# Performance work log

Measured on AMD Instinct MI355X. Metric: run time of the kernel, lower is better.

Reference implementation:

```python
import jax, jax.numpy as jnp
import numpy as np

N_EMBD = 1024
N_HEAD = 16
HEAD_DIM = N_EMBD // N_HEAD


def setup_inputs() -> dict:
    key = jax.random.key(0)
    ks = jax.random.split(key, 9)
    B, T, C = 4, 2048, N_EMBD
    s = 1.0 / np.sqrt(C)
    return {
        "x": jax.random.normal(ks[0], (B, T, C), dtype=jnp.float32),
        "Wq": jax.random.normal(ks[1], (C, C), dtype=jnp.float32) * s,
        "bq": jnp.zeros((C,), dtype=jnp.float32),
        "Wk": jax.random.normal(ks[2], (C, C), dtype=jnp.float32) * s,
        "bk": jnp.zeros((C,), dtype=jnp.float32),
        "Wv": jax.random.normal(ks[3], (C, C), dtype=jnp.float32) * s,
        "bv": jnp.zeros((C,), dtype=jnp.float32),
        "Wo": jax.random.normal(ks[4], (C, C), dtype=jnp.float32) * s,
        "bo": jnp.zeros((C,), dtype=jnp.float32),
    }


def reference(x, Wq, bq, Wk, bk, Wv, bv, Wo, bo):
    B, T, C = x.shape
    H, D = N_HEAD, HEAD_DIM
    # torch Linear: y = x @ W.T + b ; here W stored as (in, out) so y = x @ W + b
    q = (x @ Wq + bq).reshape(B, T, H, D).transpose(0, 2, 1, 3)  # [B,H,T,D]
    k = (x @ Wk + bk).reshape(B, T, H, D).transpose(0, 2, 1, 3)
    v = (x @ Wv + bv).reshape(B, T, H, D).transpose(0, 2, 1, 3)
    scores = jnp.einsum('bhqd,bhkd->bhqk', q, k) / jnp.sqrt(jnp.float32(D))
    causal = jnp.tril(jnp.ones((T, T), dtype=bool))  # [T,T]
    scores = jnp.where(causal[None, None, :, :], scores, -jnp.inf)
    weights = jax.nn.softmax(scores, axis=-1)
    # dropout disabled (eval mode / deterministic reference)
    out = jnp.einsum('bhqk,bhkd->bhqd', weights, v)  # [B,H,T,D]
    out = out.transpose(0, 2, 1, 3).reshape(B, T, C)
    return out @ Wo + bo
```

## Files before the change

kernel.cpp:

```cpp
#include <hip/hip_runtime.h>
#include <stdint.h>
#include <stddef.h>

#define NB 4
#define NT 2048
#define NC 1024
#define NH 16
#define ND 64
#define NM (NB*NT)
#define KVB 64

typedef __bf16 bf16_t;
typedef __attribute__((ext_vector_type(8)))  __bf16 bf16x8;
typedef __attribute__((ext_vector_type(4)))  __bf16 bf16x4;
typedef __attribute__((ext_vector_type(2)))  __bf16 bf16x2;
typedef __attribute__((ext_vector_type(4)))  float  f32x4;
typedef __attribute__((ext_vector_type(16))) float  f32x16;
typedef __attribute__((ext_vector_type(4)))  unsigned int u32x4;

#define QK_SCALE_LOG2E 0.18033688011112042f

__device__ __forceinline__ f32x4 mfma_bf16(bf16x8 a, bf16x8 b, f32x4 c) {
  return __builtin_amdgcn_mfma_f32_16x16x32_bf16(a, b, c, 0, 0, 0);
}
__device__ __forceinline__ f32x16 mfma32(bf16x8 a, bf16x8 b, f32x16 c) {
  return __builtin_amdgcn_mfma_f32_32x32x16_bf16(a, b, c, 0, 0, 0);
}

__device__ __forceinline__ void gld_lds16(const void* g, void* l) {
  __builtin_amdgcn_global_load_lds(
      (const __attribute__((address_space(1))) void*)g,
      (__attribute__((address_space(3))) void*)l, 16, 0, 0);
}

__device__ __forceinline__ unsigned int pack_bf16(float a, float b) {
  bf16x2 t; t[0] = (bf16_t)a; t[1] = (bf16_t)b;
  return __builtin_bit_cast(unsigned int, t);
}

#if __has_builtin(__builtin_amdgcn_permlane32_swap)
typedef __attribute__((ext_vector_type(2))) unsigned int u32x2;
__device__ __forceinline__ void plswap(unsigned int &a, unsigned int &b) {
  u32x2 r = __builtin_amdgcn_permlane32_swap(a, b, false, false);
  a = r[0]; b = r[1];
}
#else
__device__ __forceinline__ void plswap(unsigned int &a, unsigned int &b) {
  asm volatile("s_nop 1\n\tv_permlane32_swap_b32 %0, %1\n\ts_nop 1"
               : "+v"(a), "+v"(b));
}
#endif

__global__ __launch_bounds__(256) void cast_x_kernel(const float* __restrict__ x,
                                                     bf16_t* __restrict__ xb, int n4) {
  const int stride = gridDim.x * blockDim.x;
  for (int i = blockIdx.x * blockDim.x + threadIdx.x; i < n4; i += stride) {
    float4 v = reinterpret_cast<const float4*>(x)[i];
    bf16x4 o;
    o[0] = (bf16_t)v.x; o[1] = (bf16_t)v.y; o[2] = (bf16_t)v.z; o[3] = (bf16_t)v.w;
    reinterpret_cast<bf16x4*>(xb)[i] = o;
  }
}

__global__ __launch_bounds__(256) void transpose_cast_kernel(const float* __restrict__ W,
                                                             bf16_t* __restrict__ WT) {
  __shared__ float tile[32][33];
  const int t = threadIdx.x;
  const int tx = t & 31, ty = t >> 5;
  const int k0 = (blockIdx.x & 31) << 5;
  const int n0 = (blockIdx.x >> 5) << 5;
#pragma unroll
  for (int i = 0; i < 4; ++i)
    tile[ty + 8*i][tx] = W[(size_t)(k0 + ty + 8*i)*NC + n0 + tx];
  __syncthreads();
#pragma unroll
  for (int i = 0; i < 4; ++i)
    WT[(size_t)(n0 + ty + 8*i)*NC + k0 + tx] = (bf16_t)tile[tx][ty + 8*i];
}

template<int MODE>
__global__ __launch_bounds__(256) void gemm_bt_kernel(
    const bf16_t* __restrict__ A, const bf16_t* __restrict__ BT,
    int M, int N, int K,
    bf16_t* __restrict__ qo, bf16_t* __restrict__ ko, bf16_t* __restrict__ vo,
    const float* __restrict__ b0, const float* __restrict__ b1, const float* __restrict__ b2,
    float* __restrict__ outp, const float* __restrict__ bo)
{
  const int lane = threadIdx.x & 63;
  const int wv = threadIdx.x >> 6;
  const int wr = wv >> 1, wc = wv & 1;
  const int l15 = lane & 15, lg = lane >> 4;
  const int nbn = N >> 7;
  const int bm = blockIdx.x / nbn, bn = blockIdx.x % nbn;
  const int m0 = bm << 7, n0 = bn << 7;

  __shared__ char smem[32768];
  char* As = smem;
  char* Bs = smem + 16384;

  f32x4 acc[4][4] = {};

  const int nkt = K >> 6;
  for (int kt = 0; kt < nkt; ++kt) {
    const int k0 = kt << 6;
    __syncthreads();
#pragma unroll
    for (int i = 0; i < 4; ++i) {
      const int seg = i*4 + wv;
      const int lin = seg*64 + lane;
      const int row = lin >> 3;
      const int ch  = (lin & 7) ^ (row & 7);
      gld_lds16(A  + (size_t)(m0 + row)*K + k0 + (ch << 3), As + seg*1024);
      gld_lds16(BT + (size_t)(n0 + row)*K + k0 + (ch << 3), Bs + seg*1024);
    }
    __syncthreads();
#pragma unroll
    for (int ks = 0; ks < 2; ++ks) {
      bf16x8 af[4], bfr[4];
#pragma unroll
      for (int fr = 0; fr < 4; ++fr) {
        const int row = wr*64 + fr*16 + l15;
        const int ch  = (ks*4 + lg) ^ (row & 7);
        af[fr] = *reinterpret_cast<const bf16x8*>(As + row*128 + ch*16);
      }
#pragma unroll
      for (int fc = 0; fc < 4; ++fc) {
        const int row = wc*64 + fc*16 + l15;
        const int ch  = (ks*4 + lg) ^ (row & 7);
        bfr[fc] = *reinterpret_cast<const bf16x8*>(Bs + row*128 + ch*16);
      }
#pragma unroll
      for (int fr = 0; fr < 4; ++fr)
#pragma unroll
        for (int fc = 0; fc < 4; ++fc)
          acc[fr][fc] = mfma_bf16(af[fr], bfr[fc], acc[fr][fc]);
    }
  }

#pragma unroll
  for (int fr = 0; fr < 4; ++fr) {
#pragma unroll
    for (int fc = 0; fc < 4; ++fc) {
      const int mrow0 = m0 + wr*64 + fr*16 + (lg << 2);
      const int ncol  = n0 + wc*64 + fc*16 + l15;
      if (MODE == 0) {
        const int mat = ncol >> 10, c = ncol & 1023;
        const int h = c >> 6, d = c & 63;
        if (mat == 2) {
          const float bias = b2[c];
          bf16x4 ov;
#pragma unroll
          for (int r = 0; r < 4; ++r) ov[r] = (bf16_t)(acc[fr][fc][r] + bias);
          const int bb = mrow0 >> 11, tt = mrow0 & (NT - 1);
          *reinterpret_cast<bf16x4*>(vo + ((((size_t)bb*NH + h)*ND + d)*NT) + tt) = ov;
        } else {
          bf16_t* dst = (mat == 0) ? qo : ko;
          const float* bptr = (mat == 0) ? b0 : b1;
          const float bias = bptr[c];
          const float scl = (mat == 0) ? QK_SCALE_LOG2E : 1.0f;
#pragma unroll
          for (int r = 0; r < 4; ++r) {
            const int mm = mrow0 + r;
            const int bb = mm >> 11, tt = mm & (NT - 1);
            dst[((((size_t)bb*NH + h)*NT + tt) << 6) + d] =
                (bf16_t)((acc[fr][fc][r] + bias) * scl);
          }
        }
      } else {
        const float bias = bo[ncol];
#pragma unroll
        for (int r = 0; r < 4; ++r)
          outp[(size_t)(mrow0 + r)*N + ncol] = acc[fr][fc][r] + bias;
      }
    }
  }
}

__global__ __launch_bounds__(256) void attn_kernel(
    const bf16_t* __restrict__ q, const bf16_t* __restrict__ k, const bf16_t* __restrict__ vt,
    bf16_t* __restrict__ o)
{
  const int lane = threadIdx.x & 63;
  const int wv = threadIdx.x >> 6;
  const int l31 = lane & 31, h = lane >> 5;

  const int qblk = 15 - (blockIdx.x >> 6);
  const int bh   = blockIdx.x & 63;
  const int bb = bh >> 4, hh = bh & 15;
  const int q0 = qblk << 7;

  __shared__ char smem[4*8192];
  char* const ks0 = smem;
  char* const ks1 = smem + 8192;
  char* const vs0 = smem + 16384;
  char* const vs1 = smem + 24576;

  const size_t base = (size_t)bh * (NT * ND);
  const bf16_t* Kg = k  + base;
  const bf16_t* Vg = vt + base;

  const int q0w = q0 + wv*32;
  const int qg  = q0w + l31;

#pragma unroll
  for (int p = 0; p < 2; ++p) {
    const int seg = p*4 + wv, lin = seg*64 + lane;
    const int row = lin >> 3, ch = (lin & 7) ^ (row & 7);
    gld_lds16(Kg + (size_t)row*ND + (ch << 3), ks0 + seg*1024);
    gld_lds16(Vg + (size_t)row*NT + (ch << 3), vs0 + seg*1024);
  }

  bf16x8 qf[4];
  {
    const bf16_t* Qg = q + base + (size_t)qg*ND + 8*h;
#pragma unroll
    for (int ds = 0; ds < 4; ++ds)
      qf[ds] = *reinterpret_cast<const bf16x8*>(Qg + 16*ds);
  }

  bf16x8 ones8;
#pragma unroll
  for (int jj = 0; jj < 8; ++jj) ones8[jj] = (bf16_t)1.0f;

  f32x16 oc[2] = {};
  f32x16 lacc = {};

  const int nkv = 2*qblk + 2;

  for (int j = 0; j < nkv; ++j) {
    const int kt0 = j << 6;
    const bool cur1 = (j & 1) != 0;
    char* Kc = cur1 ? ks1 : ks0;
    char* Vc = cur1 ? vs1 : vs0;

    if (j + 1 < nkv) {
      char* Kn = cur1 ? ks0 : ks1;
      char* Vn = cur1 ? vs0 : vs1;
      const int nt0 = kt0 + KVB;
#pragma unroll
      for (int p = 0; p < 2; ++p) {
        const int seg = p*4 + wv, lin = seg*64 + lane;
        const int row = lin >> 3, ch = (lin & 7) ^ (row & 7);
        gld_lds16(Kg + (size_t)(nt0 + row)*ND + (ch << 3), Kn + seg*1024);
        gld_lds16(Vg + (size_t)row*NT + nt0 + (ch << 3), Vn + seg*1024);
      }
      asm volatile("s_waitcnt vmcnt(4)" ::: "memory");
    } else {
      asm volatile("s_waitcnt vmcnt(0)" ::: "memory");
    }
    __syncthreads();

    const bool active = (kt0 <= q0w + 31);
    if (active) {
      f32x16 st[2] = {};
      __builtin_amdgcn_s_setprio(1);
#pragma unroll
      for (int ds = 0; ds < 4; ++ds) {
#pragma unroll
        for (int kt = 0; kt < 2; ++kt) {
          const int row = kt*32 + l31;
          const int cl  = (2*ds + h) ^ (row & 7);
          const bf16x8 kfr = *reinterpret_cast<const bf16x8*>(Kc + row*128 + cl*16);
          st[kt] = mfma32(kfr, qf[ds], st[kt]);
        }
      }
      __builtin_amdgcn_s_setprio(0);

      const bool needmask = (kt0 + KVB - 1) > q0w;
      if (needmask) {
        const int qrel = qg - kt0 - 4*h;
#pragma unroll
        for (int kt = 0; kt < 2; ++kt)
#pragma unroll
          for (int r = 0; r < 16; ++r) {
            const int kc = (r & 3) + 8*(r >> 2) + 32*kt;
            st[kt][r] = (kc > qrel) ? 0.0f : exp2f(st[kt][r]);
          }
      } else {
#pragma unroll
        for (int kt = 0; kt < 2; ++kt)
#pragma unroll
          for (int r = 0; r < 16; ++r)
            st[kt][r] = exp2f(st[kt][r]);
      }

#pragma unroll
      for (int kt = 0; kt < 2; ++kt) {
#pragma unroll
        for (int g = 0; g < 2; ++g) {
          unsigned int wa = pack_bf16(st[kt][8*g + 0], st[kt][8*g + 1]);
          unsigned int wb = pack_bf16(st[kt][8*g + 2], st[kt][8*g + 3]);
          unsigned int wc = pack_bf16(st[kt][8*g + 4], st[kt][8*g + 5]);
          unsigned int wd = pack_bf16(st[kt][8*g + 6], st[kt][8*g + 7]);
          plswap(wa, wc);
          plswap(wb, wd);
          u32x4 pb; pb[0] = wa; pb[1] = wb; pb[2] = wc; pb[3] = wd;
          const bf16x8 pf = __builtin_bit_cast(bf16x8, pb);
          const int kg = 2*kt + g;
          __builtin_amdgcn_s_setprio(1);
          lacc = mfma32(ones8, pf, lacc);
#pragma unroll
          for (int da = 0; da < 2; ++da) {
            const int row = 32*da + l31;
            const int cl  = (2*kg + h) ^ (row & 7);
            const bf16x8 vf = *reinterpret_cast<const bf16x8*>(Vc + row*128 + cl*16);
            oc[da] = mfma32(vf, pf, oc[da]);
          }
          __builtin_amdgcn_s_setprio(0);
        }
      }
    }
    __syncthreads();
  }

  const float rl = 1.0f / lacc[0];
  bf16_t* orow = o + ((size_t)bb*NT + qg)*NC + hh*ND;
#pragma unroll
  for (int da = 0; da < 2; ++da) {
#pragma unroll
    for (int u = 0; u < 4; ++u) {
      bf16x4 ov;
#pragma unroll
      for (int jj = 0; jj < 4; ++jj) ov[jj] = (bf16_t)(oc[da][4*u + jj] * rl);
      *reinterpret_cast<bf16x4*>(orow + 32*da + 8*u + 4*h) = ov;
    }
  }
}

extern "C" void kernel_launch(void* const* d_in, const int* in_sizes, int n_in,
                              void* d_out, int out_size, void* d_ws, size_t ws_size,
                              hipStream_t stream) {
  (void)in_sizes; (void)n_in; (void)out_size;
  const float* x  = (const float*)d_in[0];
  const float* Wq = (const float*)d_in[1];
  const float* bq = (const float*)d_in[2];
  const float* Wk = (const float*)d_in[3];
  const float* bk = (const float*)d_in[4];
  const float* Wv = (const float*)d_in[5];
  const float* bv = (const float*)d_in[6];
  const float* Wo = (const float*)d_in[7];
  const float* bo = (const float*)d_in[8];
  float* out = (float*)d_out;

  const size_t off_xb    = 0;
  const size_t off_wqkvT = 16777216;
  const size_t off_woT   = 23068672;
  const size_t off_q     = 25165824;
  const size_t off_k     = 41943040;
  const size_t off_v     = 58720256;
  const size_t off_attn  = 75497472;
  const size_t need      = 92274688;
  if (ws_size < need) return;

  char* ws = (char*)d_ws;
  bf16_t* xb    = (bf16_t*)(ws + off_xb);
  bf16_t* wqkvT = (bf16_t*)(ws + off_wqkvT);
  bf16_t* woT   = (bf16_t*)(ws + off_woT);
  bf16_t* qb    = (bf16_t*)(ws + off_q);
  bf16_t* kb    = (bf16_t*)(ws + off_k);
  bf16_t* vtb   = (bf16_t*)(ws + off_v);
  bf16_t* attnb = (bf16_t*)(ws + off_attn);

  cast_x_kernel<<<dim3(2048), dim3(256), 0, stream>>>(x, xb, NM*NC/4);
  transpose_cast_kernel<<<dim3(1024), dim3(256), 0, stream>>>(Wq, wqkvT);
  transpose_cast_kernel<<<dim3(1024), dim3(256), 0, stream>>>(Wk, wqkvT + 1048576);
  transpose_cast_kernel<<<dim3(1024), dim3(256), 0, stream>>>(Wv, wqkvT + 2097152);
  transpose_cast_kernel<<<dim3(1024), dim3(256), 0, stream>>>(Wo, woT);

  gemm_bt_kernel<0><<<dim3(64*24), dim3(256), 0, stream>>>(
      xb, wqkvT, NM, 3*NC, NC, qb, kb, vtb, bq, bk, bv, nullptr, nullptr);

  attn_kernel<<<dim3(16*64), dim3(256), 0, stream>>>(qb, kb, vtb, attnb);

  gemm_bt_kernel<1><<<dim3(64*8), dim3(256), 0, stream>>>(
      attnb, woT, NM, NC, NC, nullptr, nullptr, nullptr, nullptr, nullptr, nullptr,
      out, bo);
}
```

Before: 191.0 us.

## Shrink attention blocks to 64 query rows with two waves and single barrier

```diff
diff --git a/kernel.cpp b/kernel.cpp
--- a/kernel.cpp
+++ b/kernel.cpp
@@ -176,18 +176,19 @@
   }
 }
 
-__global__ __launch_bounds__(256) void attn_kernel(
+__global__ __launch_bounds__(128) void attn_kernel(
     const bf16_t* __restrict__ q, const bf16_t* __restrict__ k, const bf16_t* __restrict__ vt,
     bf16_t* __restrict__ o)
 {
-  const int lane = threadIdx.x & 63;
-  const int wv = threadIdx.x >> 6;
-  const int l31 = lane & 31, h = lane >> 5;
-
-  const int qblk = 15 - (blockIdx.x >> 6);
+  const int tid  = threadIdx.x;
+  const int lane = tid & 63;
+  const int wv   = tid >> 6;
+  const int l31  = lane & 31, h = lane >> 5;
+
+  const int tile = 31 - (blockIdx.x >> 6);
   const int bh   = blockIdx.x & 63;
   const int bb = bh >> 4, hh = bh & 15;
-  const int q0 = qblk << 7;
+  const int q0 = tile << 6;
 
   __shared__ char smem[4*8192];
   char* const ks0 = smem;
@@ -202,12 +203,21 @@
   const int q0w = q0 + wv*32;
   const int qg  = q0w + l31;
 
-#pragma unroll
-  for (int p = 0; p < 2; ++p) {
-    const int seg = p*4 + wv, lin = seg*64 + lane;
-    const int row = lin >> 3, ch = (lin & 7) ^ (row & 7);
-    gld_lds16(Kg + (size_t)row*ND + (ch << 3), ks0 + seg*1024);
-    gld_lds16(Vg + (size_t)row*NT + (ch << 3), vs0 + seg*1024);
+  int offk[4], offv[4], segb[4];
+#pragma unroll
+  for (int p = 0; p < 4; ++p) {
+    const int c   = p*128 + tid;
+    const int row = c >> 3;
+    const int ch  = (c & 7) ^ (row & 7);
+    offk[p] = row*ND + (ch << 3);
+    offv[p] = row*NT + (ch << 3);
+    segb[p] = (p*2 + wv) * 1024;
+  }
+
+#pragma unroll
+  for (int p = 0; p < 4; ++p) {
+    gld_lds16(Kg + offk[p], ks0 + segb[p]);
+    gld_lds16(Vg + offv[p], vs0 + segb[p]);
   }
 
   bf16x8 qf[4];
@@ -225,92 +235,86 @@
   f32x16 oc[2] = {};
   f32x16 lacc = {};
 
-  const int nkv = 2*qblk + 2;
+  const int nkv = tile + 1;
 
   for (int j = 0; j < nkv; ++j) {
-    const int kt0 = j << 6;
     const bool cur1 = (j & 1) != 0;
-    char* Kc = cur1 ? ks1 : ks0;
-    char* Vc = cur1 ? vs1 : vs0;
+    char* const Kc = cur1 ? ks1 : ks0;
+    char* const Vc = cur1 ? vs1 : vs0;
+
+    asm volatile("s_waitcnt vmcnt(0)" ::: "memory");
+    __builtin_amdgcn_s_barrier();
+    __builtin_amdgcn_sched_barrier(0);
 
     if (j + 1 < nkv) {
-      char* Kn = cur1 ? ks0 : ks1;
-      char* Vn = cur1 ? vs0 : vs1;
-      const int nt0 = kt0 + KVB;
-#pragma unroll
-      for (int p = 0; p < 2; ++p) {
-        const int seg = p*4 + wv, lin = seg*64 + lane;
-        const int row = lin >> 3, ch = (lin & 7) ^ (row & 7);
-        gld_lds16(Kg + (size_t)(nt0 + row)*ND + (ch << 3), Kn + seg*1024);
-        gld_lds16(Vg + (size_t)row*NT + nt0 + (ch << 3), Vn + seg*1024);
-      }
-      asm volatile("s_waitcnt vmcnt(4)" ::: "memory");
+      char* const Kn = cur1 ? ks0 : ks1;
+      char* const Vn = cur1 ? vs0 : vs1;
+      const int kadv = (j + 1) * (KVB * ND);
+      const int vadv = (j + 1) * KVB;
+#pragma unroll
+      for (int p = 0; p < 4; ++p) {
+        gld_lds16(Kg + kadv + offk[p], Kn + segb[p]);
+        gld_lds16(Vg + vadv + offv[p], Vn + segb[p]);
+      }
+      __builtin_amdgcn_sched_barrier(0);
+    }
+
+    f32x16 st[2] = {};
+    __builtin_amdgcn_s_setprio(1);
+#pragma unroll
+    for (int ds = 0; ds < 4; ++ds) {
+#pragma unroll
+      for (int kt = 0; kt < 2; ++kt) {
+        const int row = kt*32 + l31;
+        const int cl  = (2*ds + h) ^ (row & 7);
+        const bf16x8 kfr = *reinterpret_cast<const bf16x8*>(Kc + row*128 + cl*16);
+        st[kt] = mfma32(kfr, qf[ds], st[kt]);
+      }
+    }
+    __builtin_amdgcn_s_setprio(0);
+
+    if (j == nkv - 1) {
+      const int qrel = qg - (j << 6) - 4*h;
+#pragma unroll
+      for (int kt = 0; kt < 2; ++kt)
+#pragma unroll
+        for (int r = 0; r < 16; ++r) {
+          const int kc = (r & 3) + 8*(r >> 2) + 32*kt;
+          st[kt][r] = (kc > qrel) ? 0.0f : exp2f(st[kt][r]);
+        }
     } else {
-      asm volatile("s_waitcnt vmcnt(0)" ::: "memory");
-    }
-    __syncthreads();
-
-    const bool active = (kt0 <= q0w + 31);
-    if (active) {
-      f32x16 st[2] = {};
-      __builtin_amdgcn_s_setprio(1);
-#pragma unroll
-      for (int ds = 0; ds < 4; ++ds) {
-#pragma unroll
-        for (int kt = 0; kt < 2; ++kt) {
-          const int row = kt*32 + l31;
-          const int cl  = (2*ds + h) ^ (row & 7);
-          const bf16x8 kfr = *reinterpret_cast<const bf16x8*>(Kc + row*128 + cl*16);
-          st[kt] = mfma32(kfr, qf[ds], st[kt]);
+#pragma unroll
+      for (int kt = 0; kt < 2; ++kt)
+#pragma unroll
+        for (int r = 0; r < 16; ++r)
+          st[kt][r] = exp2f(st[kt][r]);
+    }
+
+#pragma unroll
+    for (int kt = 0; kt < 2; ++kt) {
+#pragma unroll
+      for (int g = 0; g < 2; ++g) {
+        unsigned int wa = pack_bf16(st[kt][8*g + 0], st[kt][8*g + 1]);
+        unsigned int wb = pack_bf16(st[kt][8*g + 2], st[kt][8*g + 3]);
+        unsigned int wc = pack_bf16(st[kt][8*g + 4], st[kt][8*g + 5]);
+        unsigned int wd = pack_bf16(st[kt][8*g + 6], st[kt][8*g + 7]);
+        plswap(wa, wc);
+        plswap(wb, wd);
+        u32x4 pb; pb[0] = wa; pb[1] = wb; pb[2] = wc; pb[3] = wd;
+        const bf16x8 pf = __builtin_bit_cast(bf16x8, pb);
+        const int kg = 2*kt + g;
+        __builtin_amdgcn_s_setprio(1);
+        lacc = mfma32(ones8, pf, lacc);
+#pragma unroll
+        for (int da = 0; da < 2; ++da) {
+          const int row = 32*da + l31;
+          const int cl  = (2*kg + h) ^ (row & 7);
+          const bf16x8 vf = *reinterpret_cast<const bf16x8*>(Vc + row*128 + cl*16);
+          oc[da] = mfma32(vf, pf, oc[da]);
         }
-      }
-      __builtin_amdgcn_s_setprio(0);
-
-      const bool needmask = (kt0 + KVB - 1) > q0w;
-      if (needmask) {
-        const int qrel = qg - kt0 - 4*h;
-#pragma unroll
-        for (int kt = 0; kt < 2; ++kt)
-#pragma unroll
-          for (int r = 0; r < 16; ++r) {
-            const int kc = (r & 3) + 8*(r >> 2) + 32*kt;
-            st[kt][r] = (kc > qrel) ? 0.0f : exp2f(st[kt][r]);
-          }
-      } else {
-#pragma unroll
-        for (int kt = 0; kt < 2; ++kt)
-#pragma unroll
-          for (int r = 0; r < 16; ++r)
-            st[kt][r] = exp2f(st[kt][r]);
-      }
-
-#pragma unroll
-      for (int kt = 0; kt < 2; ++kt) {
-#pragma unroll
-        for (int g = 0; g < 2; ++g) {
-          unsigned int wa = pack_bf16(st[kt][8*g + 0], st[kt][8*g + 1]);
-          unsigned int wb = pack_bf16(st[kt][8*g + 2], st[kt][8*g + 3]);
-          unsigned int wc = pack_bf16(st[kt][8*g + 4], st[kt][8*g + 5]);
-          unsigned int wd = pack_bf16(st[kt][8*g + 6], st[kt][8*g + 7]);
-          plswap(wa, wc);
-          plswap(wb, wd);
-          u32x4 pb; pb[0] = wa; pb[1] = wb; pb[2] = wc; pb[3] = wd;
-          const bf16x8 pf = __builtin_bit_cast(bf16x8, pb);
-          const int kg = 2*kt + g;
-          __builtin_amdgcn_s_setprio(1);
-          lacc = mfma32(ones8, pf, lacc);
-#pragma unroll
-          for (int da = 0; da < 2; ++da) {
-            const int row = 32*da + l31;
-            const int cl  = (2*kg + h) ^ (row & 7);
-            const bf16x8 vf = *reinterpret_cast<const bf16x8*>(Vc + row*128 + cl*16);
-            oc[da] = mfma32(vf, pf, oc[da]);
-          }
-          __builtin_amdgcn_s_setprio(0);
-        }
-      }
-    }
-    __syncthreads();
+        __builtin_amdgcn_s_setprio(0);
+      }
+    }
   }
 
   const float rl = 1.0f / lacc[0];
@@ -370,7 +374,7 @@
   gemm_bt_kernel<0><<<dim3(64*24), dim3(256), 0, stream>>>(
       xb, wqkvT, NM, 3*NC, NC, qb, kb, vtb, bq, bk, bv, nullptr, nullptr);
 
-  attn_kernel<<<dim3(16*64), dim3(256), 0, stream>>>(qb, kb, vtb, attnb);
+  attn_kernel<<<dim3(32*64), dim3(128), 0, stream>>>(qb, kb, vtb, attnb);
 
   gemm_bt_kernel<1><<<dim3(64*8), dim3(256), 0, stream>>>(
       attnb, woT, NM, NC, NC, nullptr, nullptr, nullptr, nullptr, nullptr, nullptr,
```

Result: no change. 191.4 us (+0.2%).
